# Performance work log

Measured on AMD Instinct MI355X. Metric: run time of the kernel, lower is better.

The kernel has to match this reference:

```python
import jax, jax.numpy as jnp
import numpy as np

EMBED_DIM = 512
NUM_HEAD = 16
HEAD_DIM = EMBED_DIM // NUM_HEAD
EPS = 1e-6


def setup_inputs() -> dict:
    key = jax.random.key(0)
    ks = jax.random.split(key, 7)
    B, L = 4, 4096
    scale = 1.0 / np.sqrt(EMBED_DIM)
    return {
        "query": jax.random.normal(ks[0], (B, L, EMBED_DIM), jnp.float32),
        "key": jax.random.normal(ks[1], (B, L, EMBED_DIM), jnp.float32),
        "value": jax.random.normal(ks[2], (B, L, EMBED_DIM), jnp.float32),
        "Wq": jax.random.normal(ks[3], (EMBED_DIM, EMBED_DIM), jnp.float32) * scale,
        "Wk": jax.random.normal(ks[4], (EMBED_DIM, EMBED_DIM), jnp.float32) * scale,
        "Wv": jax.random.normal(ks[5], (EMBED_DIM, EMBED_DIM), jnp.float32) * scale,
        "Wm": jax.random.normal(ks[6], (EMBED_DIM, EMBED_DIM), jnp.float32) * scale,
    }


def reference(query, key, value, Wq, Wk, Wv, Wm):
    bs, Lq, E = query.shape
    H, D = NUM_HEAD, HEAD_DIM
    # projections (nn.Linear without bias: x @ W.T)
    q = (query @ Wq.T).reshape(bs, Lq, H, D)
    k = (key @ Wk.T).reshape(bs, -1, H, D)
    v = (value @ Wv.T).reshape(bs, -1, H, D)
    # elu+1 feature map
    Q = jax.nn.elu(q) + 1.0
    K = jax.nn.elu(k) + 1.0
    v_len = v.shape[1]
    v = v / v_len
    # KV accumulation: [n, h, d, dv]
    KV = jnp.einsum('nshd,nshv->nhdv', K, v)
    # normalizer Z: [n, l, h]
    Z = 1.0 / (jnp.einsum('nlhd,nhd->nlh', Q, K.sum(axis=1)) + EPS)
    # weighted combination: [n, l, h, dv]
    message = jnp.einsum('nlhd,nhdv,nlh->nlhv', Q, KV, Z) * v_len
    # merge projection (dropout p=0 -> identity)
    out = message.reshape(bs, Lq, H * D) @ Wm.T
    return out
```

## Files before the change

### kernel.cpp

```cpp
#include <hip/hip_runtime.h>

#define EMBED  512
#define NHEAD  16
#define HDIM   32
#define NBATCH 4
#define SEQ    4096
#define NROWS  (NBATCH * SEQ)
#define FEPS   1e-6f

typedef __attribute__((ext_vector_type(8))) short short8;
typedef __attribute__((ext_vector_type(4))) float f32x4;

__device__ __forceinline__ short f2bf(float x) {
    unsigned u = __float_as_uint(x);
    u += 0x7FFFu + ((u >> 16) & 1u);
    return (short)(u >> 16);
}
__device__ __forceinline__ float bf2f(short h) {
    return __uint_as_float(((unsigned)(unsigned short)h) << 16);
}

__global__ __launch_bounds__(256)
void convert_w4(const float* __restrict__ W0, const float* __restrict__ W1,
                const float* __restrict__ W2, const float* __restrict__ W3,
                short* __restrict__ H0, short* __restrict__ L0,
                short* __restrict__ H1, short* __restrict__ L1,
                short* __restrict__ H2, short* __restrict__ L2,
                short* __restrict__ H3, short* __restrict__ L3) {
    const int seg = blockIdx.x >> 8;
    const int i = ((blockIdx.x & 255) * 256 + threadIdx.x) * 4;
    const float* W = (seg == 0) ? W0 : (seg == 1) ? W1 : (seg == 2) ? W2 : W3;
    short* H = (seg == 0) ? H0 : (seg == 1) ? H1 : (seg == 2) ? H2 : H3;
    short* L = (seg == 0) ? L0 : (seg == 1) ? L1 : (seg == 2) ? L2 : L3;
    float4 v = *(const float4*)(W + i);
    short4 h, l;
    h.x = f2bf(v.x); l.x = f2bf(v.x - bf2f(h.x));
    h.y = f2bf(v.y); l.y = f2bf(v.y - bf2f(h.y));
    h.z = f2bf(v.z); l.z = f2bf(v.z - bf2f(h.z));
    h.w = f2bf(v.w); l.w = f2bf(v.w - bf2f(h.w));
    *(short4*)(H + i) = h;
    *(short4*)(L + i) = l;
}

#define LDA 40

__global__ __launch_bounds__(256, 2)
void qkv_gemm(const float* __restrict__ Aq, const float* __restrict__ Ak,
              const float* __restrict__ Av,
              const short* __restrict__ WqH, const short* __restrict__ WqL,
              const short* __restrict__ WkH, const short* __restrict__ WkL,
              const short* __restrict__ WvH, const short* __restrict__ WvL,
              float* __restrict__ Qb, float* __restrict__ Kb,
              float* __restrict__ Vb) {
    __shared__ short Ah[128][LDA];
    __shared__ short Al[128][LDA];

    const int tid  = threadIdx.x;
    const int lane = tid & 63;
    const int wave = tid >> 6;
    const int wm   = (wave >> 1) * 64;
    const int wn   = (wave & 1) * 64;
    const int l15  = lane & 15;
    const int kg   = lane >> 4;

    const int lin = blockIdx.x;
    const int op  = lin >> 9;
    const int r_  = lin & 511;
    const int bn  = (r_ >> 7) * 128;
    const int bm  = (r_ & 127) * 128;

    const float* A   = (op == 0) ? Aq  : (op == 1) ? Ak  : Av;
    const short* Whi = (op == 0) ? WqH : (op == 1) ? WkH : WvH;
    const short* Wlo = (op == 0) ? WqL : (op == 1) ? WkL : WvL;
    float* C = (op == 0) ? Qb : (op == 1) ? Kb : Vb;

    const int sr = tid >> 2;
    const int sk = (tid & 3) * 8;
    const float* Ap0 = A + (size_t)(bm + sr) * EMBED + sk;
    const float* Ap1 = Ap0 + (size_t)64 * EMBED;

    const short* Bh = Whi + (size_t)(bn + wn + l15) * EMBED + kg * 8;
    const short* Bl = Wlo + (size_t)(bn + wn + l15) * EMBED + kg * 8;

    f32x4 acc[4][4];
#pragma unroll
    for (int i = 0; i < 4; ++i)
#pragma unroll
        for (int j = 0; j < 4; ++j) acc[i][j] = (f32x4)0.0f;

#pragma unroll 1
    for (int k0 = 0; k0 < EMBED; k0 += 32) {
        float4 a0 = *(const float4*)(Ap0 + k0);
        float4 a1 = *(const float4*)(Ap0 + k0 + 4);
        float4 a2 = *(const float4*)(Ap1 + k0);
        float4 a3 = *(const float4*)(Ap1 + k0 + 4);
        short8 bh[4], bl[4];
#pragma unroll
        for (int j = 0; j < 4; ++j) {
            bh[j] = *(const short8*)(Bh + (size_t)j * 16 * EMBED + k0);
            bl[j] = *(const short8*)(Bl + (size_t)j * 16 * EMBED + k0);
        }
        __syncthreads();
        {
            float v[8] = {a0.x, a0.y, a0.z, a0.w, a1.x, a1.y, a1.z, a1.w};
            short8 hv, lv;
#pragma unroll
            for (int q = 0; q < 8; ++q) {
                short hb = f2bf(v[q]);
                hv[q] = hb; lv[q] = f2bf(v[q] - bf2f(hb));
            }
            *(short8*)&Ah[sr][sk] = hv;
            *(short8*)&Al[sr][sk] = lv;
        }
        {
            float v[8] = {a2.x, a2.y, a2.z, a2.w, a3.x, a3.y, a3.z, a3.w};
            short8 hv, lv;
#pragma unroll
            for (int q = 0; q < 8; ++q) {
                short hb = f2bf(v[q]);
                hv[q] = hb; lv[q] = f2bf(v[q] - bf2f(hb));
            }
            *(short8*)&Ah[sr + 64][sk] = hv;
            *(short8*)&Al[sr + 64][sk] = lv;
        }
        __syncthreads();

        short8 ah[4], alr[4];
#pragma unroll
        for (int i = 0; i < 4; ++i) {
            ah[i]  = *(const short8*)&Ah[wm + i * 16 + l15][kg * 8];
            alr[i] = *(const short8*)&Al[wm + i * 16 + l15][kg * 8];
        }
#pragma unroll
        for (int i = 0; i < 4; ++i)
#pragma unroll
            for (int j = 0; j < 4; ++j) {
                acc[i][j] = __builtin_amdgcn_mfma_f32_16x16x32_bf16(ah[i],  bh[j], acc[i][j], 0, 0, 0);
                acc[i][j] = __builtin_amdgcn_mfma_f32_16x16x32_bf16(ah[i],  bl[j], acc[i][j], 0, 0, 0);
                acc[i][j] = __builtin_amdgcn_mfma_f32_16x16x32_bf16(alr[i], bh[j], acc[i][j], 0, 0, 0);
            }
    }

#pragma unroll
    for (int i = 0; i < 4; ++i)
#pragma unroll
        for (int j = 0; j < 4; ++j) {
            const int col = bn + wn + j * 16 + l15;
#pragma unroll
            for (int r = 0; r < 4; ++r) {
                const int row = bm + wm + i * 16 + kg * 4 + r;
                float vv = acc[i][j][r];
                if (op < 2) vv = (vv > 0.f) ? (vv + 1.f) : __expf(vv);
                else        vv = vv * (1.0f / (float)SEQ);
                C[(size_t)row * EMBED + col] = vv;
            }
        }
}

__global__ __launch_bounds__(256, 2)
void merge_gemm(const float* __restrict__ A, const short* __restrict__ Whi,
                const short* __restrict__ Wlo, float* __restrict__ C) {
    __shared__ short Ah[128][LDA];
    __shared__ short Al[128][LDA];

    const int tid  = threadIdx.x;
    const int lane = tid & 63;
    const int wave = tid >> 6;
    const int wm   = (wave >> 1) * 64;
    const int wn   = (wave & 1) * 64;
    const int l15  = lane & 15;
    const int kg   = lane >> 4;

    const int lin = blockIdx.x;
    const int bn  = (lin >> 7) * 128;
    const int bm  = (lin & 127) * 128;

    const int sr = tid >> 2;
    const int sk = (tid & 3) * 8;
    const float* Ap0 = A + (size_t)(bm + sr) * EMBED + sk;
    const float* Ap1 = Ap0 + (size_t)64 * EMBED;

    const short* Bh = Whi + (size_t)(bn + wn + l15) * EMBED + kg * 8;
    const short* Bl = Wlo + (size_t)(bn + wn + l15) * EMBED + kg * 8;

    f32x4 acc[4][4];
#pragma unroll
    for (int i = 0; i < 4; ++i)
#pragma unroll
        for (int j = 0; j < 4; ++j) acc[i][j] = (f32x4)0.0f;

#pragma unroll 1
    for (int k0 = 0; k0 < EMBED; k0 += 32) {
        float4 a0 = *(const float4*)(Ap0 + k0);
        float4 a1 = *(const float4*)(Ap0 + k0 + 4);
        float4 a2 = *(const float4*)(Ap1 + k0);
        float4 a3 = *(const float4*)(Ap1 + k0 + 4);
        short8 bh[4], bl[4];
#pragma unroll
        for (int j = 0; j < 4; ++j) {
            bh[j] = *(const short8*)(Bh + (size_t)j * 16 * EMBED + k0);
            bl[j] = *(const short8*)(Bl + (size_t)j * 16 * EMBED + k0);
        }
        __syncthreads();
        {
            float v[8] = {a0.x, a0.y, a0.z, a0.w, a1.x, a1.y, a1.z, a1.w};
            short8 hv, lv;
#pragma unroll
            for (int q = 0; q < 8; ++q) {
                short hb = f2bf(v[q]);
                hv[q] = hb; lv[q] = f2bf(v[q] - bf2f(hb));
            }
            *(short8*)&Ah[sr][sk] = hv;
            *(short8*)&Al[sr][sk] = lv;
        }
        {
            float v[8] = {a2.x, a2.y, a2.z, a2.w, a3.x, a3.y, a3.z, a3.w};
            short8 hv, lv;
#pragma unroll
            for (int q = 0; q < 8; ++q) {
                short hb = f2bf(v[q]);
                hv[q] = hb; lv[q] = f2bf(v[q] - bf2f(hb));
            }
            *(short8*)&Ah[sr + 64][sk] = hv;
            *(short8*)&Al[sr + 64][sk] = lv;
        }
        __syncthreads();

        short8 ah[4], alr[4];
#pragma unroll
        for (int i = 0; i < 4; ++i) {
            ah[i]  = *(const short8*)&Ah[wm + i * 16 + l15][kg * 8];
            alr[i] = *(const short8*)&Al[wm + i * 16 + l15][kg * 8];
        }
#pragma unroll
        for (int i = 0; i < 4; ++i)
#pragma unroll
            for (int j = 0; j < 4; ++j) {
                acc[i][j] = __builtin_amdgcn_mfma_f32_16x16x32_bf16(ah[i],  bh[j], acc[i][j], 0, 0, 0);
                acc[i][j] = __builtin_amdgcn_mfma_f32_16x16x32_bf16(ah[i],  bl[j], acc[i][j], 0, 0, 0);
                acc[i][j] = __builtin_amdgcn_mfma_f32_16x16x32_bf16(alr[i], bh[j], acc[i][j], 0, 0, 0);
            }
    }

#pragma unroll
    for (int i = 0; i < 4; ++i)
#pragma unroll
        for (int j = 0; j < 4; ++j) {
            const int col = bn + wn + j * 16 + l15;
#pragma unroll
            for (int r = 0; r < 4; ++r) {
                const int row = bm + wm + i * 16 + kg * 4 + r;
                C[(size_t)row * EMBED + col] = acc[i][j][r];
            }
        }
}

__global__ __launch_bounds__(256)
void kv_ksum_mfma(const float* __restrict__ Kf, const float* __restrict__ Vf,
                  float* __restrict__ KV, float* __restrict__ Ksum) {
    __shared__ char smem[34816];
    short (*Kh)[34] = (short (*)[34])smem;
    short (*Kl)[34] = (short (*)[34])(smem + 8704);
    short (*Vh)[34] = (short (*)[34])(smem + 17408);
    short (*Vl)[34] = (short (*)[34])(smem + 26112);

    const int bh_ = blockIdx.y;
    const int b = bh_ >> 4, h = bh_ & 15;
    const int s0 = blockIdx.x * 256;
    const int t = threadIdx.x;
    const int lane = t & 63, wave = t >> 6;
    const int l15 = lane & 15, kg = lane >> 4;
    const int ws = wave * 32;

    const int sl = t >> 1;
    const int dsel = (t & 1) * 16;
    const float* Kbase = Kf + (size_t)b * SEQ * EMBED + h * HDIM;
    const float* Vbase = Vf + (size_t)b * SEQ * EMBED + h * HDIM;

    f32x4 kvacc[2][2], ksacc[2];
#pragma unroll
    for (int i = 0; i < 2; ++i) {
        ksacc[i] = (f32x4)0.0f;
#pragma unroll
        for (int j = 0; j < 2; ++j) kvacc[i][j] = (f32x4)0.0f;
    }
    short8 ones;
#pragma unroll
    for (int q = 0; q < 8; ++q) ones[q] = (short)0x3F80;

    float4 kx[4], vx[4];
#pragma unroll
    for (int p = 0; p < 4; ++p) {
        kx[p] = *(const float4*)(Kbase + (size_t)(s0 + sl) * EMBED + dsel + 4 * p);
        vx[p] = *(const float4*)(Vbase + (size_t)(s0 + sl) * EMBED + dsel + 4 * p);
    }

#pragma unroll 1
    for (int it = 0; it < 2; ++it) {
        __syncthreads();
        {
            float kv_[8] = {kx[0].x, kx[0].y, kx[0].z, kx[0].w, kx[1].x, kx[1].y, kx[1].z, kx[1].w};
            float kv2[8] = {kx[2].x, kx[2].y, kx[2].z, kx[2].w, kx[3].x, kx[3].y, kx[3].z, kx[3].w};
            float vv_[8] = {vx[0].x, vx[0].y, vx[0].z, vx[0].w, vx[1].x, vx[1].y, vx[1].z, vx[1].w};
            float vv2[8] = {vx[2].x, vx[2].y, vx[2].z, vx[2].w, vx[3].x, vx[3].y, vx[3].z, vx[3].w};
            short8 h0, l0, h1, l1;
#pragma unroll
            for (int q = 0; q < 8; ++q) { short hb = f2bf(kv_[q]); h0[q] = hb; l0[q] = f2bf(kv_[q] - bf2f(hb)); }
#pragma unroll
            for (int q = 0; q < 8; ++q) { short hb = f2bf(kv2[q]); h1[q] = hb; l1[q] = f2bf(kv2[q] - bf2f(hb)); }
            *(short8*)&Kh[sl][dsel] = h0; *(short8*)&Kh[sl][dsel + 8] = h1;
            *(short8*)&Kl[sl][dsel] = l0; *(short8*)&Kl[sl][dsel + 8] = l1;
#pragma unroll
            for (int q = 0; q < 8; ++q) { short hb = f2bf(vv_[q]); h0[q] = hb; l0[q] = f2bf(vv_[q] - bf2f(hb)); }
#pragma unroll
            for (int q = 0; q < 8; ++q) { short hb = f2bf(vv2[q]); h1[q] = hb; l1[q] = f2bf(vv2[q] - bf2f(hb)); }
            *(short8*)&Vh[sl][dsel] = h0; *(short8*)&Vh[sl][dsel + 8] = h1;
            *(short8*)&Vl[sl][dsel] = l0; *(short8*)&Vl[sl][dsel + 8] = l1;
        }
        __syncthreads();
        if (it == 0) {
#pragma unroll
            for (int p = 0; p < 4; ++p) {
                kx[p] = *(const float4*)(Kbase + (size_t)(s0 + 128 + sl) * EMBED + dsel + 4 * p);
                vx[p] = *(const float4*)(Vbase + (size_t)(s0 + 128 + sl) * EMBED + dsel + 4 * p);
            }
        }
        short8 kah[2], kal[2], vbh[2], vbl[2];
#pragma unroll
        for (int i = 0; i < 2; ++i) {
#pragma unroll
            for (int q = 0; q < 8; ++q) {
                const int srow = ws + kg * 8 + q;
                const int col  = i * 16 + l15;
                kah[i][q] = Kh[srow][col];
                kal[i][q] = Kl[srow][col];
                vbh[i][q] = Vh[srow][col];
                vbl[i][q] = Vl[srow][col];
            }
        }
#pragma unroll
        for (int i = 0; i < 2; ++i) {
#pragma unroll
            for (int j = 0; j < 2; ++j) {
                kvacc[i][j] = __builtin_amdgcn_mfma_f32_16x16x32_bf16(kah[i], vbh[j], kvacc[i][j], 0, 0, 0);
                kvacc[i][j] = __builtin_amdgcn_mfma_f32_16x16x32_bf16(kah[i], vbl[j], kvacc[i][j], 0, 0, 0);
                kvacc[i][j] = __builtin_amdgcn_mfma_f32_16x16x32_bf16(kal[i], vbh[j], kvacc[i][j], 0, 0, 0);
            }
            ksacc[i] = __builtin_amdgcn_mfma_f32_16x16x32_bf16(kah[i], ones, ksacc[i], 0, 0, 0);
            ksacc[i] = __builtin_amdgcn_mfma_f32_16x16x32_bf16(kal[i], ones, ksacc[i], 0, 0, 0);
        }
    }

    __syncthreads();
    float* red = (float*)smem;
    float* myred = red + wave * 1056;
#pragma unroll
    for (int i = 0; i < 2; ++i)
#pragma unroll
        for (int j = 0; j < 2; ++j)
#pragma unroll
            for (int r = 0; r < 4; ++r)
                myred[(i * 16 + kg * 4 + r) * 32 + j * 16 + l15] = kvacc[i][j][r];
    if (l15 == 0) {
#pragma unroll
        for (int i = 0; i < 2; ++i)
#pragma unroll
            for (int r = 0; r < 4; ++r)
                myred[1024 + i * 16 + kg * 4 + r] = ksacc[i][r];
    }
    __syncthreads();
    float* kvout = KV + (size_t)bh_ * 1024;
    for (int idx = t; idx < 1024; idx += 256) {
        float s4 = red[idx] + red[1056 + idx] + red[2112 + idx] + red[3168 + idx];
        atomicAdd(&kvout[idx], s4);
    }
    if (t < 32) {
        float s4 = red[1024 + t] + red[1056 + 1024 + t] + red[2112 + 1024 + t] + red[3168 + 1024 + t];
        atomicAdd(&Ksum[bh_ * 32 + t], s4);
    }
}

__global__ __launch_bounds__(512)
void message_kernel(float* __restrict__ Q, const float* __restrict__ KV,
                    const float* __restrict__ Ksum) {
    const int blk  = blockIdx.x;
    const int row0 = blk * 4;
    const int b    = row0 >> 12;
    const int t    = threadIdx.x;
    const int h    = t >> 5, e = t & 31;

    __shared__ float q[4][EMBED];
    __shared__ float ks[EMBED];
    ks[t] = Ksum[b * EMBED + t];
#pragma unroll
    for (int r = 0; r < 4; ++r) q[r][t] = Q[(size_t)(row0 + r) * EMBED + t];

    const float* kvh = KV + (size_t)(b * NHEAD + h) * HDIM * HDIM + e;
    float kc[HDIM];
#pragma unroll
    for (int d = 0; d < HDIM; ++d) kc[d] = kvh[d * HDIM];
    __syncthreads();

#pragma unroll
    for (int r = 0; r < 4; ++r) {
        float zden = FEPS, m = 0.f;
#pragma unroll
        for (int d = 0; d < HDIM; ++d) {
            float qd = q[r][h * HDIM + d];
            zden = fmaf(qd, ks[h * HDIM + d], zden);
            m    = fmaf(qd, kc[d], m);
        }
        Q[(size_t)(row0 + r) * EMBED + t] = m * ((float)SEQ / zden);
    }
}

extern "C" void kernel_launch(void* const* d_in, const int* in_sizes, int n_in,
                              void* d_out, int out_size, void* d_ws, size_t ws_size,
                              hipStream_t stream) {
    const float* query = (const float*)d_in[0];
    const float* key   = (const float*)d_in[1];
    const float* value = (const float*)d_in[2];
    const float* Wq    = (const float*)d_in[3];
    const float* Wk    = (const float*)d_in[4];
    const float* Wv    = (const float*)d_in[5];
    const float* Wm    = (const float*)d_in[6];
    float* out = (float*)d_out;

    float* ws  = (float*)d_ws;
    float* Qb  = ws;
    float* Kb  = Qb + (size_t)NROWS * EMBED;
    float* Vb  = Kb + (size_t)NROWS * EMBED;
    float* KVb = Vb + (size_t)NROWS * EMBED;
    float* KSb = KVb + 64 * 1024;
    short* wsp = (short*)(KSb + 64 * HDIM);
    const int WN = EMBED * EMBED;
    short* WqH = wsp;            short* WqL = wsp + WN;
    short* WkH = wsp + 2 * WN;   short* WkL = wsp + 3 * WN;
    short* WvH = wsp + 4 * WN;   short* WvL = wsp + 5 * WN;
    short* WmH = wsp + 6 * WN;   short* WmL = wsp + 7 * WN;

    hipMemsetAsync(KVb, 0, (64 * 1024 + 64 * HDIM) * sizeof(float), stream);

    convert_w4<<<1024, 256, 0, stream>>>(Wq, Wk, Wv, Wm,
                                         WqH, WqL, WkH, WkL,
                                         WvH, WvL, WmH, WmL);

    qkv_gemm<<<1536, 256, 0, stream>>>(query, key, value,
                                       WqH, WqL, WkH, WkL, WvH, WvL,
                                       Qb, Kb, Vb);

    kv_ksum_mfma<<<dim3(16, 64), 256, 0, stream>>>(Kb, Vb, KVb, KSb);
    message_kernel<<<NROWS / 4, 512, 0, stream>>>(Qb, KVb, KSb);

    merge_gemm<<<512, 256, 0, stream>>>(Qb, WmH, WmL, out);
}
```

Baseline: 329.9 us.

## Emit K/V as transposed bf16 hi/lo splits from the GEMM epilogue

The QKV GEMM epilogue now writes K and V transposed (feature-major) as split bf16 hi/lo arrays instead of fp32 row-major. The KV/Ksum reduction kernel can then load MFMA operands straight from global memory without shared-memory staging, conversion or barriers, and it uses half as many blocks, each covering more sequence. Each MFMA group is also regrouped so independent accumulators are issued back to back. The risk is that the transposed epilogue stores are narrow and strided, which may hurt the GEMM's write efficiency.

After: 336.9 us. 2.1% more time.

```diff
diff --git a/kernel.cpp b/kernel.cpp
--- a/kernel.cpp
+++ b/kernel.cpp
@@ -50,8 +50,9 @@
               const short* __restrict__ WqH, const short* __restrict__ WqL,
               const short* __restrict__ WkH, const short* __restrict__ WkL,
               const short* __restrict__ WvH, const short* __restrict__ WvL,
-              float* __restrict__ Qb, float* __restrict__ Kb,
-              float* __restrict__ Vb) {
+              float* __restrict__ Qb,
+              short* __restrict__ KtH, short* __restrict__ KtL,
+              short* __restrict__ VtH, short* __restrict__ VtL) {
     __shared__ short Ah[128][LDA];
     __shared__ short Al[128][LDA];
 
@@ -72,7 +73,6 @@
     const float* A   = (op == 0) ? Aq  : (op == 1) ? Ak  : Av;
     const short* Whi = (op == 0) ? WqH : (op == 1) ? WkH : WvH;
     const short* Wlo = (op == 0) ? WqL : (op == 1) ? WkL : WvL;
-    float* C = (op == 0) ? Qb : (op == 1) ? Kb : Vb;
 
     const int sr = tid >> 2;
     const int sk = (tid & 3) * 8;
@@ -134,27 +134,57 @@
 #pragma unroll
         for (int i = 0; i < 4; ++i)
 #pragma unroll
+            for (int j = 0; j < 4; ++j)
+                acc[i][j] = __builtin_amdgcn_mfma_f32_16x16x32_bf16(ah[i], bh[j], acc[i][j], 0, 0, 0);
+#pragma unroll
+        for (int i = 0; i < 4; ++i)
+#pragma unroll
+            for (int j = 0; j < 4; ++j)
+                acc[i][j] = __builtin_amdgcn_mfma_f32_16x16x32_bf16(ah[i], bl[j], acc[i][j], 0, 0, 0);
+#pragma unroll
+        for (int i = 0; i < 4; ++i)
+#pragma unroll
+            for (int j = 0; j < 4; ++j)
+                acc[i][j] = __builtin_amdgcn_mfma_f32_16x16x32_bf16(alr[i], bh[j], acc[i][j], 0, 0, 0);
+    }
+
+    if (op == 0) {
+#pragma unroll
+        for (int i = 0; i < 4; ++i)
+#pragma unroll
             for (int j = 0; j < 4; ++j) {
-                acc[i][j] = __builtin_amdgcn_mfma_f32_16x16x32_bf16(ah[i],  bh[j], acc[i][j], 0, 0, 0);
-                acc[i][j] = __builtin_amdgcn_mfma_f32_16x16x32_bf16(ah[i],  bl[j], acc[i][j], 0, 0, 0);
-                acc[i][j] = __builtin_amdgcn_mfma_f32_16x16x32_bf16(alr[i], bh[j], acc[i][j], 0, 0, 0);
-            }
-    }
-
-#pragma unroll
-    for (int i = 0; i < 4; ++i)
-#pragma unroll
-        for (int j = 0; j < 4; ++j) {
-            const int col = bn + wn + j * 16 + l15;
-#pragma unroll
-            for (int r = 0; r < 4; ++r) {
-                const int row = bm + wm + i * 16 + kg * 4 + r;
-                float vv = acc[i][j][r];
-                if (op < 2) vv = (vv > 0.f) ? (vv + 1.f) : __expf(vv);
-                else        vv = vv * (1.0f / (float)SEQ);
-                C[(size_t)row * EMBED + col] = vv;
-            }
-        }
+                const int col = bn + wn + j * 16 + l15;
+#pragma unroll
+                for (int r = 0; r < 4; ++r) {
+                    const int row = bm + wm + i * 16 + kg * 4 + r;
+                    float vv = acc[i][j][r];
+                    vv = (vv > 0.f) ? (vv + 1.f) : __expf(vv);
+                    Qb[(size_t)row * EMBED + col] = vv;
+                }
+            }
+    } else {
+        short* TH = (op == 1) ? KtH : VtH;
+        short* TL = (op == 1) ? KtL : VtL;
+#pragma unroll
+        for (int i = 0; i < 4; ++i)
+#pragma unroll
+            for (int j = 0; j < 4; ++j) {
+                const int col  = bn + wn + j * 16 + l15;
+                const int rowb = bm + wm + i * 16 + kg * 4;
+                ushort4 hi4, lo4;
+#pragma unroll
+                for (int r = 0; r < 4; ++r) {
+                    float vv = acc[i][j][r];
+                    if (op == 1) vv = (vv > 0.f) ? (vv + 1.f) : __expf(vv);
+                    else         vv = vv * (1.0f / (float)SEQ);
+                    short hb = f2bf(vv);
+                    ((unsigned short*)&hi4)[r] = (unsigned short)hb;
+                    ((unsigned short*)&lo4)[r] = (unsigned short)f2bf(vv - bf2f(hb));
+                }
+                *(ushort4*)(TH + (size_t)col * NROWS + rowb) = hi4;
+                *(ushort4*)(TL + (size_t)col * NROWS + rowb) = lo4;
+            }
+    }
 }
 
 __global__ __launch_bounds__(256, 2)
@@ -235,11 +265,18 @@
 #pragma unroll
         for (int i = 0; i < 4; ++i)
 #pragma unroll
-            for (int j = 0; j < 4; ++j) {
-                acc[i][j] = __builtin_amdgcn_mfma_f32_16x16x32_bf16(ah[i],  bh[j], acc[i][j], 0, 0, 0);
-                acc[i][j] = __builtin_amdgcn_mfma_f32_16x16x32_bf16(ah[i],  bl[j], acc[i][j], 0, 0, 0);
+            for (int j = 0; j < 4; ++j)
+                acc[i][j] = __builtin_amdgcn_mfma_f32_16x16x32_bf16(ah[i], bh[j], acc[i][j], 0, 0, 0);
+#pragma unroll
+        for (int i = 0; i < 4; ++i)
+#pragma unroll
+            for (int j = 0; j < 4; ++j)
+                acc[i][j] = __builtin_amdgcn_mfma_f32_16x16x32_bf16(ah[i], bl[j], acc[i][j], 0, 0, 0);
+#pragma unroll
+        for (int i = 0; i < 4; ++i)
+#pragma unroll
+            for (int j = 0; j < 4; ++j)
                 acc[i][j] = __builtin_amdgcn_mfma_f32_16x16x32_bf16(alr[i], bh[j], acc[i][j], 0, 0, 0);
-            }
     }
 
 #pragma unroll
@@ -256,26 +293,18 @@
 }
 
 __global__ __launch_bounds__(256)
-void kv_ksum_mfma(const float* __restrict__ Kf, const float* __restrict__ Vf,
-                  float* __restrict__ KV, float* __restrict__ Ksum) {
-    __shared__ char smem[34816];
-    short (*Kh)[34] = (short (*)[34])smem;
-    short (*Kl)[34] = (short (*)[34])(smem + 8704);
-    short (*Vh)[34] = (short (*)[34])(smem + 17408);
-    short (*Vl)[34] = (short (*)[34])(smem + 26112);
+void kv_ksum_t(const short* __restrict__ KtH, const short* __restrict__ KtL,
+               const short* __restrict__ VtH, const short* __restrict__ VtL,
+               float* __restrict__ KV, float* __restrict__ Ksum) {
+    __shared__ float red[4 * 1056];
 
     const int bh_ = blockIdx.y;
     const int b = bh_ >> 4, h = bh_ & 15;
-    const int s0 = blockIdx.x * 256;
     const int t = threadIdx.x;
     const int lane = t & 63, wave = t >> 6;
     const int l15 = lane & 15, kg = lane >> 4;
-    const int ws = wave * 32;
-
-    const int sl = t >> 1;
-    const int dsel = (t & 1) * 16;
-    const float* Kbase = Kf + (size_t)b * SEQ * EMBED + h * HDIM;
-    const float* Vbase = Vf + (size_t)b * SEQ * EMBED + h * HDIM;
+
+    const int sbase = b * SEQ + blockIdx.x * 512 + wave * 128;
 
     f32x4 kvacc[2][2], ksacc[2];
 #pragma unroll
@@ -288,71 +317,43 @@
 #pragma unroll
     for (int q = 0; q < 8; ++q) ones[q] = (short)0x3F80;
 
-    float4 kx[4], vx[4];
-#pragma unroll
-    for (int p = 0; p < 4; ++p) {
-        kx[p] = *(const float4*)(Kbase + (size_t)(s0 + sl) * EMBED + dsel + 4 * p);
-        vx[p] = *(const float4*)(Vbase + (size_t)(s0 + sl) * EMBED + dsel + 4 * p);
-    }
-
-#pragma unroll 1
-    for (int it = 0; it < 2; ++it) {
-        __syncthreads();
-        {
-            float kv_[8] = {kx[0].x, kx[0].y, kx[0].z, kx[0].w, kx[1].x, kx[1].y, kx[1].z, kx[1].w};
-            float kv2[8] = {kx[2].x, kx[2].y, kx[2].z, kx[2].w, kx[3].x, kx[3].y, kx[3].z, kx[3].w};
-            float vv_[8] = {vx[0].x, vx[0].y, vx[0].z, vx[0].w, vx[1].x, vx[1].y, vx[1].z, vx[1].w};
-            float vv2[8] = {vx[2].x, vx[2].y, vx[2].z, vx[2].w, vx[3].x, vx[3].y, vx[3].z, vx[3].w};
-            short8 h0, l0, h1, l1;
-#pragma unroll
-            for (int q = 0; q < 8; ++q) { short hb = f2bf(kv_[q]); h0[q] = hb; l0[q] = f2bf(kv_[q] - bf2f(hb)); }
-#pragma unroll
-            for (int q = 0; q < 8; ++q) { short hb = f2bf(kv2[q]); h1[q] = hb; l1[q] = f2bf(kv2[q] - bf2f(hb)); }
-            *(short8*)&Kh[sl][dsel] = h0; *(short8*)&Kh[sl][dsel + 8] = h1;
-            *(short8*)&Kl[sl][dsel] = l0; *(short8*)&Kl[sl][dsel + 8] = l1;
-#pragma unroll
-            for (int q = 0; q < 8; ++q) { short hb = f2bf(vv_[q]); h0[q] = hb; l0[q] = f2bf(vv_[q] - bf2f(hb)); }
-#pragma unroll
-            for (int q = 0; q < 8; ++q) { short hb = f2bf(vv2[q]); h1[q] = hb; l1[q] = f2bf(vv2[q] - bf2f(hb)); }
-            *(short8*)&Vh[sl][dsel] = h0; *(short8*)&Vh[sl][dsel + 8] = h1;
-            *(short8*)&Vl[sl][dsel] = l0; *(short8*)&Vl[sl][dsel + 8] = l1;
-        }
-        __syncthreads();
-        if (it == 0) {
-#pragma unroll
-            for (int p = 0; p < 4; ++p) {
-                kx[p] = *(const float4*)(Kbase + (size_t)(s0 + 128 + sl) * EMBED + dsel + 4 * p);
-                vx[p] = *(const float4*)(Vbase + (size_t)(s0 + 128 + sl) * EMBED + dsel + 4 * p);
-            }
-        }
+    size_t rbase[2];
+#pragma unroll
+    for (int i = 0; i < 2; ++i)
+        rbase[i] = (size_t)(h * HDIM + i * 16 + l15) * NROWS + sbase + kg * 8;
+
+#pragma unroll 2
+    for (int s = 0; s < 128; s += 32) {
         short8 kah[2], kal[2], vbh[2], vbl[2];
 #pragma unroll
         for (int i = 0; i < 2; ++i) {
-#pragma unroll
-            for (int q = 0; q < 8; ++q) {
-                const int srow = ws + kg * 8 + q;
-                const int col  = i * 16 + l15;
-                kah[i][q] = Kh[srow][col];
-                kal[i][q] = Kl[srow][col];
-                vbh[i][q] = Vh[srow][col];
-                vbl[i][q] = Vl[srow][col];
-            }
-        }
+            kah[i] = *(const short8*)(KtH + rbase[i] + s);
+            kal[i] = *(const short8*)(KtL + rbase[i] + s);
+            vbh[i] = *(const short8*)(VtH + rbase[i] + s);
+            vbl[i] = *(const short8*)(VtL + rbase[i] + s);
+        }
+#pragma unroll
+        for (int i = 0; i < 2; ++i)
+#pragma unroll
+            for (int j = 0; j < 2; ++j)
+                kvacc[i][j] = __builtin_amdgcn_mfma_f32_16x16x32_bf16(kah[i], vbh[j], kvacc[i][j], 0, 0, 0);
+#pragma unroll
+        for (int i = 0; i < 2; ++i)
+#pragma unroll
+            for (int j = 0; j < 2; ++j)
+                kvacc[i][j] = __builtin_amdgcn_mfma_f32_16x16x32_bf16(kah[i], vbl[j], kvacc[i][j], 0, 0, 0);
+#pragma unroll
+        for (int i = 0; i < 2; ++i)
+#pragma unroll
+            for (int j = 0; j < 2; ++j)
+                kvacc[i][j] = __builtin_amdgcn_mfma_f32_16x16x32_bf16(kal[i], vbh[j], kvacc[i][j], 0, 0, 0);
 #pragma unroll
         for (int i = 0; i < 2; ++i) {
-#pragma unroll
-            for (int j = 0; j < 2; ++j) {
-                kvacc[i][j] = __builtin_amdgcn_mfma_f32_16x16x32_bf16(kah[i], vbh[j], kvacc[i][j], 0, 0, 0);
-                kvacc[i][j] = __builtin_amdgcn_mfma_f32_16x16x32_bf16(kah[i], vbl[j], kvacc[i][j], 0, 0, 0);
-                kvacc[i][j] = __builtin_amdgcn_mfma_f32_16x16x32_bf16(kal[i], vbh[j], kvacc[i][j], 0, 0, 0);
-            }
             ksacc[i] = __builtin_amdgcn_mfma_f32_16x16x32_bf16(kah[i], ones, ksacc[i], 0, 0, 0);
             ksacc[i] = __builtin_amdgcn_mfma_f32_16x16x32_bf16(kal[i], ones, ksacc[i], 0, 0, 0);
         }
     }
 
-    __syncthreads();
-    float* red = (float*)smem;
     float* myred = red + wave * 1056;
 #pragma unroll
     for (int i = 0; i < 2; ++i)
@@ -426,11 +427,14 @@
     const float* Wm    = (const float*)d_in[6];
     float* out = (float*)d_out;
 
+    const size_t S = (size_t)NROWS * EMBED;
     float* ws  = (float*)d_ws;
     float* Qb  = ws;
-    float* Kb  = Qb + (size_t)NROWS * EMBED;
-    float* Vb  = Kb + (size_t)NROWS * EMBED;
-    float* KVb = Vb + (size_t)NROWS * EMBED;
+    short* KtH = (short*)(Qb + S);
+    short* KtL = KtH + S;
+    short* VtH = KtL + S;
+    short* VtL = VtH + S;
+    float* KVb = (float*)(VtL + S);
     float* KSb = KVb + 64 * 1024;
     short* wsp = (short*)(KSb + 64 * HDIM);
     const int WN = EMBED * EMBED;
@@ -447,9 +451,9 @@
 
     qkv_gemm<<<1536, 256, 0, stream>>>(query, key, value,
                                        WqH, WqL, WkH, WkL, WvH, WvL,
-                                       Qb, Kb, Vb);
-
-    kv_ksum_mfma<<<dim3(16, 64), 256, 0, stream>>>(Kb, Vb, KVb, KSb);
+                                       Qb, KtH, KtL, VtH, VtL);
+
+    kv_ksum_t<<<dim3(8, 64), 256, 0, stream>>>(KtH, KtL, VtH, VtL, KVb, KSb);
     message_kernel<<<NROWS / 4, 512, 0, stream>>>(Qb, KVb, KSb);
 
     merge_gemm<<<512, 256, 0, stream>>>(Qb, WmH, WmL, out);
```
